# Optimization experiments

Hardware: AMD Instinct MI355X
Metric: run time of the kernel (lower is better)

Reference implementation:

```python
import jax, jax.numpy as jnp
import numpy as np

B, N, C_IN = 4, 8192, 64
NPOINT, NSAMPLE = 2048, 32
RADIUS = 0.8


def fps(xyz, npoint):
    """Furthest point sampling. xyz: (B, N, 3) -> (B, npoint) int32 indices."""
    b, n, _ = xyz.shape
    init_idx = jnp.zeros((b,), jnp.int32)
    dists0 = jnp.full((b, n), 1e10, xyz.dtype)

    def body(carry, _):
        dists, last = carry
        p = xyz[jnp.arange(b), last]                      # (B, 3) last selected point
        d = jnp.sum((xyz - p[:, None, :]) ** 2, axis=-1)  # (B, N)
        dists = jnp.minimum(dists, d)
        nxt = jnp.argmax(dists, axis=-1).astype(jnp.int32)
        return (dists, nxt), nxt

    (_, _), rest = jax.lax.scan(body, (dists0, init_idx), None, length=npoint - 1)
    return jnp.concatenate([init_idx[None, :], rest], axis=0).T  # (B, npoint)


def setup_inputs() -> dict:
    key = jax.random.key(0)
    k = jax.random.split(key, 4)
    xyz = jax.random.normal(k[0], (B, N, 3), jnp.float32) * 3.0   # point coords
    features = jax.random.normal(k[1], (B, C_IN, N), jnp.float32)
    w1 = jax.random.normal(k[2], (128, C_IN + 3), jnp.float32) * 0.05
    b1 = jnp.zeros((128,), jnp.float32)
    w2 = jax.random.normal(k[3], (256, 128), jnp.float32) * 0.05
    b2 = jnp.zeros((256,), jnp.float32)
    return {"xyz": xyz, "features": features, "w1": w1, "b1": b1, "w2": w2, "b2": b2}


def reference(xyz, features, w1, b1, w2, b2):
    b, n, _ = xyz.shape
    # --- d-fps sampling + gather_operation(new_xyz) ---
    idx_fps = fps(xyz, NPOINT)                                  # (B, S)
    new_xyz = jax.vmap(lambda p, i: p[i])(xyz, idx_fps)         # (B, S, 3)

    # --- ball query (QueryAndGroup): first NSAMPLE points within RADIUS ---
    d2 = jnp.sum((new_xyz[:, :, None, :] - xyz[:, None, :, :]) ** 2, -1)  # (B, S, N)
    in_ball = d2 < RADIUS ** 2
    idx_cnt = jnp.sum(in_ball, axis=-1)                          # (B, S)
    score = jnp.where(in_ball, jnp.arange(n, dtype=jnp.int32), n)
    neg_vals, _ = jax.lax.top_k(-score, NSAMPLE)
    idx = -neg_vals                                              # (B, S, ns) smallest valid indices
    valid = idx < n
    first = jnp.where(valid[..., :1], idx[..., :1], 0)           # pad empties with first hit (or 0)
    idx = jnp.where(valid, idx, first)

    # --- group: relative xyz concat features (use_xyz=True) ---
    gxyz = jax.vmap(lambda p, i: p[i])(xyz, idx)                 # (B, S, ns, 3)
    rel = (gxyz - new_xyz[:, :, None, :]).transpose(0, 3, 1, 2)  # (B, 3, S, ns)
    gfeat = jax.vmap(lambda f, i: f[:, i])(features, idx)        # (B, C, S, ns)
    g = jnp.concatenate([rel, gfeat], axis=1)                    # (B, C+3, S, ns)
    g = g * (idx_cnt > 0).astype(g.dtype)[:, None, :, None]      # zero empty balls

    # --- shared point MLP (1x1 conv stack) + max pool over samples ---
    h = jax.nn.relu(jnp.einsum('oc,bcsn->bosn', w1, g) + b1[None, :, None, None])
    h = jax.nn.relu(jnp.einsum('oc,bcsn->bosn', w2, h) + b2[None, :, None, None])
    pooled = jnp.max(h, axis=-1)                                 # (B, 256, S)
    return new_xyz, pooled
```

## Files before the change

### kernel.cpp

```cpp
#include <hip/hip_runtime.h>

#define NPTS   8192
#define NPT    2048
#define NS     32
#define CIN    64
#define BATCH  4
#define R2     0.64f

__global__ __launch_bounds__(256) void prep_kernel(const float* __restrict__ w1,
                                                   const float* __restrict__ w2,
                                                   float* __restrict__ w1t,
                                                   float* __restrict__ w2t) {
  int i = blockIdx.x * 256 + threadIdx.x;
  if (i < 128 * 67) {
    int o = i / 67, c = i % 67;
    w1t[c * 128 + o] = w1[i];
  }
  if (i < 256 * 128) {
    int o = i >> 7, c = i & 127;
    w2t[c * 256 + o] = w2[i];
  }
}

__global__ __launch_bounds__(256) void prep_t_kernel(const float* __restrict__ feat,
                                                     float* __restrict__ FT) {
  const int b = blockIdx.x >> 7;
  const int n0 = (blockIdx.x & 127) << 6;
  const int tid = threadIdx.x;
  __shared__ float T[64][65];

  const float* F = feat + (size_t)b * CIN * NPTS;
#pragma unroll
  for (int p = 0; p < 16; ++p) {
    int c = p * 4 + (tid >> 6), ln = tid & 63;
    T[c][ln] = F[(size_t)c * NPTS + n0 + ln];
  }
  __syncthreads();
  float* O = FT + (size_t)b * NPTS * CIN;
#pragma unroll
  for (int p = 0; p < 4; ++p) {
    int j = tid >> 2, q = (tid & 3) + p * 4;
    float4 v = make_float4(T[q * 4 + 0][j], T[q * 4 + 1][j],
                           T[q * 4 + 2][j], T[q * 4 + 3][j]);
    *(float4*)&O[(size_t)(n0 + j) * CIN + q * 4] = v;
  }
}

__device__ inline uint32_t part1by2(uint32_t x) {
  x &= 1023u;
  x = (x | (x << 16)) & 0x030000FFu;
  x = (x | (x << 8))  & 0x0300F00Fu;
  x = (x | (x << 4))  & 0x030C30C3u;
  x = (x | (x << 2))  & 0x09249249u;
  return x;
}

__device__ inline uint32_t morton3(float x, float y, float z) {
  int qx = (int)((x + 16.f) * 32.f);
  int qy = (int)((y + 16.f) * 32.f);
  int qz = (int)((z + 16.f) * 32.f);
  qx = qx < 0 ? 0 : (qx > 1023 ? 1023 : qx);
  qy = qy < 0 ? 0 : (qy > 1023 ? 1023 : qy);
  qz = qz < 0 ? 0 : (qz > 1023 ? 1023 : qz);
  return part1by2((uint32_t)qx) | (part1by2((uint32_t)qy) << 1) | (part1by2((uint32_t)qz) << 2);
}

__global__ __launch_bounds__(1024) void sort_kernel(const float* __restrict__ xyz,
                                                    float4* __restrict__ sorted) {
  const int b = blockIdx.x;
  const int tid = threadIdx.x;
  const float* X = xyz + (size_t)b * NPTS * 3;
  __shared__ uint32_t S[NPTS];

  for (int k = 0; k < 8; ++k) {
    int p = tid + (k << 10);
    uint32_t m = morton3(X[p * 3 + 0], X[p * 3 + 1], X[p * 3 + 2]);
    S[p] = ((m >> 11) << 13) | (uint32_t)p;
  }
  __syncthreads();
  for (unsigned k = 2; k <= NPTS; k <<= 1) {
    for (unsigned j = k >> 1; j > 0; j >>= 1) {
      for (int i = tid; i < NPTS; i += 1024) {
        int l = i ^ (int)j;
        if (l > i) {
          uint32_t a = S[i], c = S[l];
          bool sw = ((i & k) == 0) ? (a > c) : (a < c);
          if (sw) { S[i] = c; S[l] = a; }
        }
      }
      __syncthreads();
    }
  }
  for (int k = 0; k < 8; ++k) {
    int pos = tid + (k << 10);
    int o = (int)(S[pos] & 8191u);
    float4 v;
    v.x = X[o * 3 + 0]; v.y = X[o * 3 + 1]; v.z = X[o * 3 + 2];
    v.w = __int_as_float(o);
    sorted[(size_t)b * NPTS + pos] = v;
  }
}


#define DPP_ROR_U32_MAX(v)                                                       \
  {                                                                              \
    uint32_t _t;                                                                 \
    _t = (uint32_t)__builtin_amdgcn_update_dpp(0, (int)(v), 0x121, 0xF, 0xF, false); if (_t > (v)) (v) = _t; \
    _t = (uint32_t)__builtin_amdgcn_update_dpp(0, (int)(v), 0x122, 0xF, 0xF, false); if (_t > (v)) (v) = _t; \
    _t = (uint32_t)__builtin_amdgcn_update_dpp(0, (int)(v), 0x124, 0xF, 0xF, false); if (_t > (v)) (v) = _t; \
    _t = (uint32_t)__builtin_amdgcn_update_dpp(0, (int)(v), 0x128, 0xF, 0xF, false); if (_t > (v)) (v) = _t; \
  }

#define DPP_ROR_U32_MIN(v)                                                       \
  {                                                                              \
    uint32_t _t;                                                                 \
    _t = (uint32_t)__builtin_amdgcn_update_dpp(-1, (int)(v), 0x121, 0xF, 0xF, false); if (_t < (v)) (v) = _t; \
    _t = (uint32_t)__builtin_amdgcn_update_dpp(-1, (int)(v), 0x122, 0xF, 0xF, false); if (_t < (v)) (v) = _t; \
    _t = (uint32_t)__builtin_amdgcn_update_dpp(-1, (int)(v), 0x124, 0xF, 0xF, false); if (_t < (v)) (v) = _t; \
    _t = (uint32_t)__builtin_amdgcn_update_dpp(-1, (int)(v), 0x128, 0xF, 0xF, false); if (_t < (v)) (v) = _t; \
  }

#define CSWAP(i, j)                                                              \
  if (oid[i] > oid[j]) {                                                         \
    int _ti = oid[i]; oid[i] = oid[j]; oid[j] = _ti;                             \
    float _tf;                                                                   \
    _tf = px[i]; px[i] = px[j]; px[j] = _tf;                                     \
    _tf = py[i]; py[i] = py[j]; py[j] = _tf;                                     \
    _tf = pz[i]; pz[i] = pz[j]; pz[j] = _tf;                                     \
  }

__global__ __launch_bounds__(1024) void fps_kernel(const float* __restrict__ xyz,
                                                   const float4* __restrict__ sorted,
                                                   float* __restrict__ new_xyz) {
  const int b = blockIdx.x;
  const int tid = threadIdx.x;
  const int lane = tid & 63;
  const int wv = tid >> 6;
  const float* X = xyz + (size_t)b * NPTS * 3;
  const float4* SP = sorted + (size_t)b * NPTS;

  __shared__ float XL[NPTS * 3];
  __shared__ __align__(8) uint2 rec[2][16];

  for (int i = tid; i < NPTS * 3; i += 1024) XL[i] = X[i];

  float px[8], py[8], pz[8], dmin[8];
  int oid[8];
#pragma unroll
  for (int k = 0; k < 8; ++k) {
    float4 p = SP[tid * 8 + k];
    px[k] = p.x; py[k] = p.y; pz[k] = p.z;
    oid[k] = __float_as_int(p.w);
    dmin[k] = 1e10f;
  }
  CSWAP(0, 1) CSWAP(2, 3) CSWAP(4, 5) CSWAP(6, 7)
  CSWAP(0, 2) CSWAP(1, 3) CSWAP(4, 6) CSWAP(5, 7)
  CSWAP(1, 2) CSWAP(5, 6)
  CSWAP(0, 4) CSWAP(1, 5) CSWAP(2, 6) CSWAP(3, 7)
  CSWAP(2, 4) CSWAP(3, 5)
  CSWAP(1, 2) CSWAP(3, 4) CSWAP(5, 6)

  float bxmin = px[0], bxmax = px[0], bymin = py[0], bymax = py[0], bzmin = pz[0], bzmax = pz[0];
#pragma unroll
  for (int k = 1; k < 8; ++k) {
    bxmin = fminf(bxmin, px[k]); bxmax = fmaxf(bxmax, px[k]);
    bymin = fminf(bymin, py[k]); bymax = fmaxf(bymax, py[k]);
    bzmin = fminf(bzmin, pz[k]); bzmax = fmaxf(bzmax, pz[k]);
  }
  float cmaxv = 1e10f;
  int   cmaxi = oid[0];
  uint32_t wwm = 0u, wwi = 0u;

  float cx = X[0], cy = X[1], cz = X[2];
  if (tid == 0) {
    new_xyz[(size_t)b * NPT * 3 + 0] = cx;
    new_xyz[(size_t)b * NPT * 3 + 1] = cy;
    new_xyz[(size_t)b * NPT * 3 + 2] = cz;
  }
  __syncthreads();

  for (int t = 1; t < NPT; ++t) {
    float ex = fmaxf(fmaxf(bxmin - cx, cx - bxmax), 0.f);
    float ey = fmaxf(fmaxf(bymin - cy, cy - bymax), 0.f);
    float ez = fmaxf(fmaxf(bzmin - cz, cz - bzmax), 0.f);
    float dlb = (ex * ex + ey * ey + ez * ez) * 0.9999f;
    bool act = dlb < cmaxv;

    if (__ballot(act)) {
      if (act) {
        float mv = -1.0f; int mi = 0;
#pragma unroll
        for (int k = 0; k < 8; ++k) {
          float dx = px[k] - cx, dy = py[k] - cy, dz = pz[k] - cz;
          float d = __fadd_rn(__fadd_rn(__fmul_rn(dx, dx), __fmul_rn(dy, dy)), __fmul_rn(dz, dz));
          float dm = fminf(dmin[k], d);
          dmin[k] = dm;
          if (dm > mv) { mv = dm; mi = oid[k]; }
        }
        cmaxv = mv; cmaxi = mi;
      }
      uint32_t vb = __float_as_uint(cmaxv);
      uint32_t rm = vb;
      DPP_ROR_U32_MAX(rm)
      uint32_t m0 = (uint32_t)__builtin_amdgcn_readlane((int)rm, 0);
      uint32_t m1 = (uint32_t)__builtin_amdgcn_readlane((int)rm, 16);
      uint32_t m2 = (uint32_t)__builtin_amdgcn_readlane((int)rm, 32);
      uint32_t m3 = (uint32_t)__builtin_amdgcn_readlane((int)rm, 48);
      uint32_t wm = m0 > m1 ? m0 : m1;
      uint32_t wmb = m2 > m3 ? m2 : m3;
      wm = wm > wmb ? wm : wmb;
      unsigned long long em = __ballot(vb == wm);
      uint32_t wi;
      if (__popcll(em) == 1) {
        wi = (uint32_t)__builtin_amdgcn_readlane(cmaxi, __ffsll(em) - 1);
      } else {
        uint32_t ik = (vb == wm) ? (uint32_t)cmaxi : 0xFFFFFFFFu;
        DPP_ROR_U32_MIN(ik)
        uint32_t i0 = (uint32_t)__builtin_amdgcn_readlane((int)ik, 0);
        uint32_t i1 = (uint32_t)__builtin_amdgcn_readlane((int)ik, 16);
        uint32_t i2 = (uint32_t)__builtin_amdgcn_readlane((int)ik, 32);
        uint32_t i3 = (uint32_t)__builtin_amdgcn_readlane((int)ik, 48);
        wi = i0 < i1 ? i0 : i1;
        uint32_t wib = i2 < i3 ? i2 : i3;
        wi = wi < wib ? wi : wib;
      }
      wwm = wm; wwi = wi;
    }

    const int buf = t & 1;
    if (lane == 0) { rec[buf][wv].x = wwm; rec[buf][wv].y = wwi; }
    __syncthreads();

    uint2 r = rec[buf][lane & 15];
    uint32_t bm = r.x;
    DPP_ROR_U32_MAX(bm)
    uint32_t ci = (r.x == bm) ? r.y : 0xFFFFFFFFu;
    DPP_ROR_U32_MIN(ci)
    int sidx = __builtin_amdgcn_readfirstlane((int)ci);

    cx = XL[3 * sidx + 0];
    cy = XL[3 * sidx + 1];
    cz = XL[3 * sidx + 2];

    if (tid == 0) {
      float* o = new_xyz + ((size_t)b * NPT + t) * 3;
      o[0] = cx; o[1] = cy; o[2] = cz;
    }
  }
}

__global__ __launch_bounds__(256) void ballquery_kernel(const float* __restrict__ xyz,
                                                        const float* __restrict__ new_xyz,
                                                        int* __restrict__ idx_out) {
  const int w = blockIdx.x * 4 + (threadIdx.x >> 6);
  const int lane = threadIdx.x & 63;
  const int b = w >> 11;
  const float* X = xyz + (size_t)b * NPTS * 3;
  const float cx = new_xyz[w * 3 + 0];
  const float cy = new_xyz[w * 3 + 1];
  const float cz = new_xyz[w * 3 + 2];
  int* out = idx_out + (size_t)w * NS;

  int found = 0;
  int first = -1;
  for (int base = 0; base < NPTS; base += 64) {
    const int p = base + lane;
    float x = X[p * 3 + 0], y = X[p * 3 + 1], z = X[p * 3 + 2];
    float dx = x - cx, dy = y - cy, dz = z - cz;
    float d2 = __fadd_rn(__fadd_rn(__fmul_rn(dx, dx), __fmul_rn(dy, dy)), __fmul_rn(dz, dz));
    unsigned long long mask = __ballot(d2 < R2);
    if (mask != 0ull && first < 0) first = base + __ffsll((unsigned long long)mask) - 1;
    if (found < NS) {
      if ((mask >> lane) & 1ull) {
        int rank = found + __popcll(mask & ((1ull << lane) - 1ull));
        if (rank < NS) out[rank] = p;
      }
    }
    found += __popcll(mask);
    if (found >= NS) break;
  }
  if (found < NS) {
    int pad = (first < 0) ? 0 : first;
    if (lane >= found && lane < NS) out[lane] = pad;
  }
}

__global__ __launch_bounds__(512) void group_mlp_kernel(const float* __restrict__ xyz,
                                                        const float* __restrict__ FT,
                                                        const float* __restrict__ new_xyz,
                                                        const int* __restrict__ idx,
                                                        const float* __restrict__ w1t,
                                                        const float* __restrict__ b1,
                                                        const float* __restrict__ w2t,
                                                        const float* __restrict__ b2,
                                                        float* __restrict__ pooled) {
  const int blk = blockIdx.x;
  const int b = blk >> 10;
  const int sin0 = (2 * blk) & 2047;
  const int tid = threadIdx.x;

  __shared__ __align__(16) float G[67 * 64];
  __shared__ __align__(16) float H1[128 * 64];
  __shared__ int   lidx[2 * NS];
  __shared__ float ctr[6];

  if (tid < 64) lidx[tid] = idx[(size_t)(2 * blk) * NS + tid];
  if (tid < 6)  ctr[tid] = new_xyz[(size_t)(2 * blk) * 3 + tid];
  __syncthreads();

  const float* Fp = FT + (size_t)b * NPTS * CIN;
  const float* X = xyz + (size_t)b * NPTS * 3;

  {
    int j = tid >> 3, q = tid & 7;
    int p = lidx[j];
    const float4* row = (const float4*)(Fp + (size_t)p * CIN);
    float4 v0 = row[q * 2 + 0];
    float4 v1 = row[q * 2 + 1];
    float vs[8] = {v0.x, v0.y, v0.z, v0.w, v1.x, v1.y, v1.z, v1.w};
#pragma unroll
    for (int i = 0; i < 8; ++i)
      G[(3 + q * 8 + i) * 64 + j] = vs[i];
  }
  if (tid < 192) {
    int c = tid >> 6, j = tid & 63;
    int p = lidx[j];
    G[c * 64 + j] = X[p * 3 + c] - ctr[(j >> 5) * 3 + c];
  }
  __syncthreads();

  {
    const int oi = tid >> 4, ji = tid & 15;
    const int o0 = oi * 4, j0 = ji * 4;
    float acc[4][4];
#pragma unroll
    for (int i = 0; i < 4; ++i)
#pragma unroll
      for (int jj = 0; jj < 4; ++jj) acc[i][jj] = 0.f;
#pragma unroll 4
    for (int c = 0; c < 67; ++c) {
      float4 g  = *(const float4*)&G[c * 64 + j0];
      float4 wf = *(const float4*)&w1t[c * 128 + o0];
      float ga[4] = {g.x, g.y, g.z, g.w};
      float wa[4] = {wf.x, wf.y, wf.z, wf.w};
#pragma unroll
      for (int i = 0; i < 4; ++i)
#pragma unroll
        for (int jj = 0; jj < 4; ++jj)
          acc[i][jj] = fmaf(wa[i], ga[jj], acc[i][jj]);
    }
    float4 bb = *(const float4*)&b1[o0];
    float ba[4] = {bb.x, bb.y, bb.z, bb.w};
#pragma unroll
    for (int i = 0; i < 4; ++i) {
      float4 h;
      h.x = fmaxf(acc[i][0] + ba[i], 0.f);
      h.y = fmaxf(acc[i][1] + ba[i], 0.f);
      h.z = fmaxf(acc[i][2] + ba[i], 0.f);
      h.w = fmaxf(acc[i][3] + ba[i], 0.f);
      *(float4*)&H1[(o0 + i) * 64 + j0] = h;
    }
  }
  __syncthreads();

  {
    const int oi = tid >> 4, ji = tid & 15;
    const int o0 = oi * 8, j0 = ji * 4;
    float acc[8][4];
#pragma unroll
    for (int i = 0; i < 8; ++i)
#pragma unroll
      for (int jj = 0; jj < 4; ++jj) acc[i][jj] = 0.f;
#pragma unroll 2
    for (int c = 0; c < 128; ++c) {
      float4 h  = *(const float4*)&H1[c * 64 + j0];
      float4 wa4 = *(const float4*)&w2t[c * 256 + o0];
      float4 wb4 = *(const float4*)&w2t[c * 256 + o0 + 4];
      float ha[4] = {h.x, h.y, h.z, h.w};
      float wa[8] = {wa4.x, wa4.y, wa4.z, wa4.w, wb4.x, wb4.y, wb4.z, wb4.w};
#pragma unroll
      for (int i = 0; i < 8; ++i)
#pragma unroll
        for (int jj = 0; jj < 4; ++jj)
          acc[i][jj] = fmaf(wa[i], ha[jj], acc[i][jj]);
    }
    float4 b2a = *(const float4*)&b2[o0];
    float4 b2b = *(const float4*)&b2[o0 + 4];
    float bb[8] = {b2a.x, b2a.y, b2a.z, b2a.w, b2b.x, b2b.y, b2b.z, b2b.w};
    float m[8];
#pragma unroll
    for (int i = 0; i < 8; ++i) {
      float v0 = fmaxf(acc[i][0] + bb[i], 0.f);
      float v1 = fmaxf(acc[i][1] + bb[i], 0.f);
      float v2 = fmaxf(acc[i][2] + bb[i], 0.f);
      float v3 = fmaxf(acc[i][3] + bb[i], 0.f);
      m[i] = fmaxf(fmaxf(v0, v1), fmaxf(v2, v3));
    }
#pragma unroll
    for (int off = 1; off < 8; off <<= 1)
#pragma unroll
      for (int i = 0; i < 8; ++i) m[i] = fmaxf(m[i], __shfl_xor(m[i], off));
    const int ji_ = tid & 15;
    if (ji_ == 0 || ji_ == 8) {
      int sidx = sin0 + (ji_ >> 3);
#pragma unroll
      for (int i = 0; i < 8; ++i)
        pooled[((size_t)b * 256 + o0 + i) * (size_t)NPT + sidx] = m[i];
    }
  }
}

extern "C" void kernel_launch(void* const* d_in, const int* in_sizes, int n_in,
                              void* d_out, int out_size, void* d_ws, size_t ws_size,
                              hipStream_t stream) {
  (void)in_sizes; (void)n_in; (void)out_size; (void)ws_size;
  const float* xyz  = (const float*)d_in[0];
  const float* feat = (const float*)d_in[1];
  const float* w1   = (const float*)d_in[2];
  const float* b1   = (const float*)d_in[3];
  const float* w2   = (const float*)d_in[4];
  const float* b2   = (const float*)d_in[5];

  float* out     = (float*)d_out;
  float* new_xyz = out;
  float* pooled  = out + (size_t)BATCH * NPT * 3;

  char* ws = (char*)d_ws;
  float*  w1t    = (float*)ws;
  float*  w2t    = (float*)(ws + 34304);
  int*    idx    = (int*)(ws + 34304 + 131072);
  float4* sorted = (float4*)(ws + 1213952);
  float*  FT     = (float*)(ws + 1738240);

  prep_kernel<<<128, 256, 0, stream>>>(w1, w2, w1t, w2t);
  prep_t_kernel<<<BATCH * 128, 256, 0, stream>>>(feat, FT);
  sort_kernel<<<BATCH, 1024, 0, stream>>>(xyz, sorted);
  fps_kernel<<<BATCH, 1024, 0, stream>>>(xyz, sorted, new_xyz);
  ballquery_kernel<<<(BATCH * NPT) / 4, 256, 0, stream>>>(xyz, new_xyz, idx);
  group_mlp_kernel<<<(BATCH * NPT) / 2, 512, 0, stream>>>(xyz, FT, new_xyz, idx,
                                                          w1t, b1, w2t, b2, pooled);
}
```

Measured before the change: 1.923 ms.

## Fuse FPS, ball query and MLP into persistent kernel with progress flags

Replaces the separate FPS, ball-query and group-MLP kernels with one persistent kernel. Four blocks run FPS and publish progress every 16 samples through release atomics. The other 252 worker blocks poll those counters, then do ball query and the MLP for groups of 4 centroids, so this work overlaps the serial FPS loop. The design relies on all 256 blocks being co-resident (one 1024-thread block per CU), and the spin-waits plus the larger per-block tile add risk and can change occupancy.

```diff
diff --git a/kernel.cpp b/kernel.cpp
--- a/kernel.cpp
+++ b/kernel.cpp
@@ -6,6 +6,9 @@
 #define CIN    64
 #define BATCH  4
 #define R2     0.64f
+
+#define NWORK  252
+#define NQUAD  2048
 
 __global__ __launch_bounds__(256) void prep_kernel(const float* __restrict__ w1,
                                                    const float* __restrict__ w2,
@@ -129,283 +132,281 @@
     _tf = pz[i]; pz[i] = pz[j]; pz[j] = _tf;                                     \
   }
 
-__global__ __launch_bounds__(1024) void fps_kernel(const float* __restrict__ xyz,
-                                                   const float4* __restrict__ sorted,
-                                                   float* __restrict__ new_xyz) {
-  const int b = blockIdx.x;
+__global__ __launch_bounds__(1024, 1) void fused_kernel(
+    const float* __restrict__ xyz, const float4* __restrict__ sorted,
+    const float* __restrict__ FT,
+    const float* __restrict__ w1t, const float* __restrict__ b1,
+    const float* __restrict__ w2t, const float* __restrict__ b2,
+    float* __restrict__ new_xyz, float* __restrict__ pooled,
+    int* __restrict__ progress) {
   const int tid = threadIdx.x;
   const int lane = tid & 63;
   const int wv = tid >> 6;
-  const float* X = xyz + (size_t)b * NPTS * 3;
-  const float4* SP = sorted + (size_t)b * NPTS;
-
-  __shared__ float XL[NPTS * 3];
-  __shared__ __align__(8) uint2 rec[2][16];
-
-  for (int i = tid; i < NPTS * 3; i += 1024) XL[i] = X[i];
-
-  float px[8], py[8], pz[8], dmin[8];
-  int oid[8];
-#pragma unroll
-  for (int k = 0; k < 8; ++k) {
-    float4 p = SP[tid * 8 + k];
-    px[k] = p.x; py[k] = p.y; pz[k] = p.z;
-    oid[k] = __float_as_int(p.w);
-    dmin[k] = 1e10f;
-  }
-  CSWAP(0, 1) CSWAP(2, 3) CSWAP(4, 5) CSWAP(6, 7)
-  CSWAP(0, 2) CSWAP(1, 3) CSWAP(4, 6) CSWAP(5, 7)
-  CSWAP(1, 2) CSWAP(5, 6)
-  CSWAP(0, 4) CSWAP(1, 5) CSWAP(2, 6) CSWAP(3, 7)
-  CSWAP(2, 4) CSWAP(3, 5)
-  CSWAP(1, 2) CSWAP(3, 4) CSWAP(5, 6)
-
-  float bxmin = px[0], bxmax = px[0], bymin = py[0], bymax = py[0], bzmin = pz[0], bzmax = pz[0];
-#pragma unroll
-  for (int k = 1; k < 8; ++k) {
-    bxmin = fminf(bxmin, px[k]); bxmax = fmaxf(bxmax, px[k]);
-    bymin = fminf(bymin, py[k]); bymax = fmaxf(bymax, py[k]);
-    bzmin = fminf(bzmin, pz[k]); bzmax = fmaxf(bzmax, pz[k]);
-  }
-  float cmaxv = 1e10f;
-  int   cmaxi = oid[0];
-  uint32_t wwm = 0u, wwi = 0u;
-
-  float cx = X[0], cy = X[1], cz = X[2];
-  if (tid == 0) {
-    new_xyz[(size_t)b * NPT * 3 + 0] = cx;
-    new_xyz[(size_t)b * NPT * 3 + 1] = cy;
-    new_xyz[(size_t)b * NPT * 3 + 2] = cz;
-  }
-  __syncthreads();
-
-  for (int t = 1; t < NPT; ++t) {
-    float ex = fmaxf(fmaxf(bxmin - cx, cx - bxmax), 0.f);
-    float ey = fmaxf(fmaxf(bymin - cy, cy - bymax), 0.f);
-    float ez = fmaxf(fmaxf(bzmin - cz, cz - bzmax), 0.f);
-    float dlb = (ex * ex + ey * ey + ez * ez) * 0.9999f;
-    bool act = dlb < cmaxv;
-
-    if (__ballot(act)) {
-      if (act) {
-        float mv = -1.0f; int mi = 0;
-#pragma unroll
-        for (int k = 0; k < 8; ++k) {
-          float dx = px[k] - cx, dy = py[k] - cy, dz = pz[k] - cz;
-          float d = __fadd_rn(__fadd_rn(__fmul_rn(dx, dx), __fmul_rn(dy, dy)), __fmul_rn(dz, dz));
-          float dm = fminf(dmin[k], d);
-          dmin[k] = dm;
-          if (dm > mv) { mv = dm; mi = oid[k]; }
-        }
-        cmaxv = mv; cmaxi = mi;
-      }
-      uint32_t vb = __float_as_uint(cmaxv);
-      uint32_t rm = vb;
-      DPP_ROR_U32_MAX(rm)
-      uint32_t m0 = (uint32_t)__builtin_amdgcn_readlane((int)rm, 0);
-      uint32_t m1 = (uint32_t)__builtin_amdgcn_readlane((int)rm, 16);
-      uint32_t m2 = (uint32_t)__builtin_amdgcn_readlane((int)rm, 32);
-      uint32_t m3 = (uint32_t)__builtin_amdgcn_readlane((int)rm, 48);
-      uint32_t wm = m0 > m1 ? m0 : m1;
-      uint32_t wmb = m2 > m3 ? m2 : m3;
-      wm = wm > wmb ? wm : wmb;
-      unsigned long long em = __ballot(vb == wm);
-      uint32_t wi;
-      if (__popcll(em) == 1) {
-        wi = (uint32_t)__builtin_amdgcn_readlane(cmaxi, __ffsll(em) - 1);
-      } else {
-        uint32_t ik = (vb == wm) ? (uint32_t)cmaxi : 0xFFFFFFFFu;
-        DPP_ROR_U32_MIN(ik)
-        uint32_t i0 = (uint32_t)__builtin_amdgcn_readlane((int)ik, 0);
-        uint32_t i1 = (uint32_t)__builtin_amdgcn_readlane((int)ik, 16);
-        uint32_t i2 = (uint32_t)__builtin_amdgcn_readlane((int)ik, 32);
-        uint32_t i3 = (uint32_t)__builtin_amdgcn_readlane((int)ik, 48);
-        wi = i0 < i1 ? i0 : i1;
-        uint32_t wib = i2 < i3 ? i2 : i3;
-        wi = wi < wib ? wi : wib;
-      }
-      wwm = wm; wwi = wi;
-    }
-
-    const int buf = t & 1;
-    if (lane == 0) { rec[buf][wv].x = wwm; rec[buf][wv].y = wwi; }
+
+  __shared__ __align__(16) char SM[100416];
+
+  if (blockIdx.x < 4) {
+    const int b = blockIdx.x;
+    float* XL = (float*)SM;
+    uint2 (*rec)[16] = (uint2(*)[16])(SM + 98304);
+    const float* X = xyz + (size_t)b * NPTS * 3;
+    const float4* SP = sorted + (size_t)b * NPTS;
+
+    for (int i = tid; i < NPTS * 3; i += 1024) XL[i] = X[i];
+
+    float px[8], py[8], pz[8], dmin[8];
+    int oid[8];
+#pragma unroll
+    for (int k = 0; k < 8; ++k) {
+      float4 p = SP[tid * 8 + k];
+      px[k] = p.x; py[k] = p.y; pz[k] = p.z;
+      oid[k] = __float_as_int(p.w);
+      dmin[k] = 1e10f;
+    }
+    CSWAP(0, 1) CSWAP(2, 3) CSWAP(4, 5) CSWAP(6, 7)
+    CSWAP(0, 2) CSWAP(1, 3) CSWAP(4, 6) CSWAP(5, 7)
+    CSWAP(1, 2) CSWAP(5, 6)
+    CSWAP(0, 4) CSWAP(1, 5) CSWAP(2, 6) CSWAP(3, 7)
+    CSWAP(2, 4) CSWAP(3, 5)
+    CSWAP(1, 2) CSWAP(3, 4) CSWAP(5, 6)
+
+    float bxmin = px[0], bxmax = px[0], bymin = py[0], bymax = py[0], bzmin = pz[0], bzmax = pz[0];
+#pragma unroll
+    for (int k = 1; k < 8; ++k) {
+      bxmin = fminf(bxmin, px[k]); bxmax = fmaxf(bxmax, px[k]);
+      bymin = fminf(bymin, py[k]); bymax = fmaxf(bymax, py[k]);
+      bzmin = fminf(bzmin, pz[k]); bzmax = fmaxf(bzmax, pz[k]);
+    }
+    float cmaxv = 1e10f;
+    int   cmaxi = oid[0];
+    uint32_t wwm = 0u, wwi = 0u;
+
+    float cx = X[0], cy = X[1], cz = X[2];
+    if (tid == 0) {
+      new_xyz[(size_t)b * NPT * 3 + 0] = cx;
+      new_xyz[(size_t)b * NPT * 3 + 1] = cy;
+      new_xyz[(size_t)b * NPT * 3 + 2] = cz;
+    }
     __syncthreads();
 
-    uint2 r = rec[buf][lane & 15];
-    uint32_t bm = r.x;
-    DPP_ROR_U32_MAX(bm)
-    uint32_t ci = (r.x == bm) ? r.y : 0xFFFFFFFFu;
-    DPP_ROR_U32_MIN(ci)
-    int sidx = __builtin_amdgcn_readfirstlane((int)ci);
-
-    cx = XL[3 * sidx + 0];
-    cy = XL[3 * sidx + 1];
-    cz = XL[3 * sidx + 2];
-
-    if (tid == 0) {
-      float* o = new_xyz + ((size_t)b * NPT + t) * 3;
-      o[0] = cx; o[1] = cy; o[2] = cz;
-    }
-  }
-}
-
-__global__ __launch_bounds__(256) void ballquery_kernel(const float* __restrict__ xyz,
-                                                        const float* __restrict__ new_xyz,
-                                                        int* __restrict__ idx_out) {
-  const int w = blockIdx.x * 4 + (threadIdx.x >> 6);
-  const int lane = threadIdx.x & 63;
-  const int b = w >> 11;
-  const float* X = xyz + (size_t)b * NPTS * 3;
-  const float cx = new_xyz[w * 3 + 0];
-  const float cy = new_xyz[w * 3 + 1];
-  const float cz = new_xyz[w * 3 + 2];
-  int* out = idx_out + (size_t)w * NS;
-
-  int found = 0;
-  int first = -1;
-  for (int base = 0; base < NPTS; base += 64) {
-    const int p = base + lane;
-    float x = X[p * 3 + 0], y = X[p * 3 + 1], z = X[p * 3 + 2];
-    float dx = x - cx, dy = y - cy, dz = z - cz;
-    float d2 = __fadd_rn(__fadd_rn(__fmul_rn(dx, dx), __fmul_rn(dy, dy)), __fmul_rn(dz, dz));
-    unsigned long long mask = __ballot(d2 < R2);
-    if (mask != 0ull && first < 0) first = base + __ffsll((unsigned long long)mask) - 1;
-    if (found < NS) {
-      if ((mask >> lane) & 1ull) {
-        int rank = found + __popcll(mask & ((1ull << lane) - 1ull));
-        if (rank < NS) out[rank] = p;
-      }
-    }
-    found += __popcll(mask);
-    if (found >= NS) break;
-  }
-  if (found < NS) {
-    int pad = (first < 0) ? 0 : first;
-    if (lane >= found && lane < NS) out[lane] = pad;
-  }
-}
-
-__global__ __launch_bounds__(512) void group_mlp_kernel(const float* __restrict__ xyz,
-                                                        const float* __restrict__ FT,
-                                                        const float* __restrict__ new_xyz,
-                                                        const int* __restrict__ idx,
-                                                        const float* __restrict__ w1t,
-                                                        const float* __restrict__ b1,
-                                                        const float* __restrict__ w2t,
-                                                        const float* __restrict__ b2,
-                                                        float* __restrict__ pooled) {
-  const int blk = blockIdx.x;
-  const int b = blk >> 10;
-  const int sin0 = (2 * blk) & 2047;
-  const int tid = threadIdx.x;
-
-  __shared__ __align__(16) float G[67 * 64];
-  __shared__ __align__(16) float H1[128 * 64];
-  __shared__ int   lidx[2 * NS];
-  __shared__ float ctr[6];
-
-  if (tid < 64) lidx[tid] = idx[(size_t)(2 * blk) * NS + tid];
-  if (tid < 6)  ctr[tid] = new_xyz[(size_t)(2 * blk) * 3 + tid];
-  __syncthreads();
-
-  const float* Fp = FT + (size_t)b * NPTS * CIN;
-  const float* X = xyz + (size_t)b * NPTS * 3;
-
-  {
-    int j = tid >> 3, q = tid & 7;
-    int p = lidx[j];
-    const float4* row = (const float4*)(Fp + (size_t)p * CIN);
-    float4 v0 = row[q * 2 + 0];
-    float4 v1 = row[q * 2 + 1];
-    float vs[8] = {v0.x, v0.y, v0.z, v0.w, v1.x, v1.y, v1.z, v1.w};
-#pragma unroll
-    for (int i = 0; i < 8; ++i)
-      G[(3 + q * 8 + i) * 64 + j] = vs[i];
-  }
-  if (tid < 192) {
-    int c = tid >> 6, j = tid & 63;
-    int p = lidx[j];
-    G[c * 64 + j] = X[p * 3 + c] - ctr[(j >> 5) * 3 + c];
-  }
-  __syncthreads();
-
-  {
-    const int oi = tid >> 4, ji = tid & 15;
-    const int o0 = oi * 4, j0 = ji * 4;
-    float acc[4][4];
-#pragma unroll
-    for (int i = 0; i < 4; ++i)
-#pragma unroll
-      for (int jj = 0; jj < 4; ++jj) acc[i][jj] = 0.f;
+    for (int t = 1; t < NPT; ++t) {
+      float ex = fmaxf(fmaxf(bxmin - cx, cx - bxmax), 0.f);
+      float ey = fmaxf(fmaxf(bymin - cy, cy - bymax), 0.f);
+      float ez = fmaxf(fmaxf(bzmin - cz, cz - bzmax), 0.f);
+      float dlb = (ex * ex + ey * ey + ez * ez) * 0.9999f;
+      bool act = dlb < cmaxv;
+
+      if (__ballot(act)) {
+        if (act) {
+          float mv = -1.0f; int mi = 0;
+#pragma unroll
+          for (int k = 0; k < 8; ++k) {
+            float dx = px[k] - cx, dy = py[k] - cy, dz = pz[k] - cz;
+            float d = __fadd_rn(__fadd_rn(__fmul_rn(dx, dx), __fmul_rn(dy, dy)), __fmul_rn(dz, dz));
+            float dm = fminf(dmin[k], d);
+            dmin[k] = dm;
+            if (dm > mv) { mv = dm; mi = oid[k]; }
+          }
+          cmaxv = mv; cmaxi = mi;
+        }
+        uint32_t vb = __float_as_uint(cmaxv);
+        uint32_t rm = vb;
+        DPP_ROR_U32_MAX(rm)
+        uint32_t m0 = (uint32_t)__builtin_amdgcn_readlane((int)rm, 0);
+        uint32_t m1 = (uint32_t)__builtin_amdgcn_readlane((int)rm, 16);
+        uint32_t m2 = (uint32_t)__builtin_amdgcn_readlane((int)rm, 32);
+        uint32_t m3 = (uint32_t)__builtin_amdgcn_readlane((int)rm, 48);
+        uint32_t wm = m0 > m1 ? m0 : m1;
+        uint32_t wmb = m2 > m3 ? m2 : m3;
+        wm = wm > wmb ? wm : wmb;
+        unsigned long long em = __ballot(vb == wm);
+        uint32_t wi;
+        if (__popcll(em) == 1) {
+          wi = (uint32_t)__builtin_amdgcn_readlane(cmaxi, __ffsll(em) - 1);
+        } else {
+          uint32_t ik = (vb == wm) ? (uint32_t)cmaxi : 0xFFFFFFFFu;
+          DPP_ROR_U32_MIN(ik)
+          uint32_t i0 = (uint32_t)__builtin_amdgcn_readlane((int)ik, 0);
+          uint32_t i1 = (uint32_t)__builtin_amdgcn_readlane((int)ik, 16);
+          uint32_t i2 = (uint32_t)__builtin_amdgcn_readlane((int)ik, 32);
+          uint32_t i3 = (uint32_t)__builtin_amdgcn_readlane((int)ik, 48);
+          wi = i0 < i1 ? i0 : i1;
+          uint32_t wib = i2 < i3 ? i2 : i3;
+          wi = wi < wib ? wi : wib;
+        }
+        wwm = wm; wwi = wi;
+      }
+
+      const int buf = t & 1;
+      if (lane == 0) { rec[buf][wv].x = wwm; rec[buf][wv].y = wwi; }
+      __syncthreads();
+
+      uint2 r = rec[buf][lane & 15];
+      uint32_t bm = r.x;
+      DPP_ROR_U32_MAX(bm)
+      uint32_t ci = (r.x == bm) ? r.y : 0xFFFFFFFFu;
+      DPP_ROR_U32_MIN(ci)
+      int sidx = __builtin_amdgcn_readfirstlane((int)ci);
+
+      cx = XL[3 * sidx + 0];
+      cy = XL[3 * sidx + 1];
+      cz = XL[3 * sidx + 2];
+
+      if (tid == 0) {
+        float* o = new_xyz + ((size_t)b * NPT + t) * 3;
+        o[0] = cx; o[1] = cy; o[2] = cz;
+        if ((t & 15) == 15)
+          __hip_atomic_store(progress + b, t, __ATOMIC_RELEASE, __HIP_MEMORY_SCOPE_AGENT);
+      }
+    }
+  } else {
+    float* G    = (float*)SM;
+    float* H1   = (float*)(SM + 34304);
+    int*   lidx = (int*)(SM + 99840);
+    float* ctr  = (float*)(SM + 100352);
+
+    const int wbid = blockIdx.x - 4;
+
+    for (int qg = wbid; qg < NQUAD; qg += NWORK) {
+      const int b = qg & 3;
+      const int s0 = (qg >> 2) * 4;
+      const float* X  = xyz + (size_t)b * NPTS * 3;
+      const float* Fp = FT + (size_t)b * NPTS * CIN;
+
+      if (tid == 0) {
+        while (__hip_atomic_load(progress + b, __ATOMIC_ACQUIRE, __HIP_MEMORY_SCOPE_AGENT) < s0 + 3)
+          __builtin_amdgcn_s_sleep(2);
+      }
+      __syncthreads();
+
+      if (tid < 12) ctr[tid] = new_xyz[((size_t)b * NPT + s0) * 3 + tid];
+      if (wv < 4) {
+        const int s = s0 + wv;
+        const float cx = new_xyz[((size_t)b * NPT + s) * 3 + 0];
+        const float cy = new_xyz[((size_t)b * NPT + s) * 3 + 1];
+        const float cz = new_xyz[((size_t)b * NPT + s) * 3 + 2];
+        int* out = lidx + wv * NS;
+        int found = 0;
+        int first = -1;
+        for (int base = 0; base < NPTS; base += 64) {
+          const int p = base + lane;
+          float x = X[p * 3 + 0], y = X[p * 3 + 1], z = X[p * 3 + 2];
+          float dx = x - cx, dy = y - cy, dz = z - cz;
+          float d2 = __fadd_rn(__fadd_rn(__fmul_rn(dx, dx), __fmul_rn(dy, dy)), __fmul_rn(dz, dz));
+          unsigned long long mask = __ballot(d2 < R2);
+          if (mask != 0ull && first < 0) first = base + __ffsll((unsigned long long)mask) - 1;
+          if (found < NS) {
+            if ((mask >> lane) & 1ull) {
+              int rank = found + __popcll(mask & ((1ull << lane) - 1ull));
+              if (rank < NS) out[rank] = p;
+            }
+          }
+          found += __popcll(mask);
+          if (found >= NS) break;
+        }
+        if (found < NS) {
+          int pad = (first < 0) ? 0 : first;
+          if (lane >= found && lane < NS) out[lane] = pad;
+        }
+      }
+      __syncthreads();
+
+      {
+        int j = tid >> 3, q = tid & 7;
+        int p = lidx[j];
+        const float4* row = (const float4*)(Fp + (size_t)p * CIN);
+        float4 v0 = row[q * 2 + 0];
+        float4 v1 = row[q * 2 + 1];
+        float vs[8] = {v0.x, v0.y, v0.z, v0.w, v1.x, v1.y, v1.z, v1.w};
+#pragma unroll
+        for (int i = 0; i < 8; ++i)
+          G[(3 + q * 8 + i) * 128 + j] = vs[i];
+      }
+      if (tid < 384) {
+        int c = tid >> 7, j = tid & 127;
+        int p = lidx[j];
+        G[c * 128 + j] = X[p * 3 + c] - ctr[(j >> 5) * 3 + c];
+      }
+      __syncthreads();
+
+      {
+        const int oi = tid >> 5, ji = tid & 31;
+        const int o0 = oi * 4, j0 = ji * 4;
+        float acc[4][4];
+#pragma unroll
+        for (int i = 0; i < 4; ++i)
+#pragma unroll
+          for (int jj = 0; jj < 4; ++jj) acc[i][jj] = 0.f;
 #pragma unroll 4
-    for (int c = 0; c < 67; ++c) {
-      float4 g  = *(const float4*)&G[c * 64 + j0];
-      float4 wf = *(const float4*)&w1t[c * 128 + o0];
-      float ga[4] = {g.x, g.y, g.z, g.w};
-      float wa[4] = {wf.x, wf.y, wf.z, wf.w};
-#pragma unroll
-      for (int i = 0; i < 4; ++i)
-#pragma unroll
-        for (int jj = 0; jj < 4; ++jj)
-          acc[i][jj] = fmaf(wa[i], ga[jj], acc[i][jj]);
-    }
-    float4 bb = *(const float4*)&b1[o0];
-    float ba[4] = {bb.x, bb.y, bb.z, bb.w};
-#pragma unroll
-    for (int i = 0; i < 4; ++i) {
-      float4 h;
-      h.x = fmaxf(acc[i][0] + ba[i], 0.f);
-      h.y = fmaxf(acc[i][1] + ba[i], 0.f);
-      h.z = fmaxf(acc[i][2] + ba[i], 0.f);
-      h.w = fmaxf(acc[i][3] + ba[i], 0.f);
-      *(float4*)&H1[(o0 + i) * 64 + j0] = h;
-    }
-  }
-  __syncthreads();
-
-  {
-    const int oi = tid >> 4, ji = tid & 15;
-    const int o0 = oi * 8, j0 = ji * 4;
-    float acc[8][4];
-#pragma unroll
-    for (int i = 0; i < 8; ++i)
-#pragma unroll
-      for (int jj = 0; jj < 4; ++jj) acc[i][jj] = 0.f;
+        for (int c = 0; c < 67; ++c) {
+          float4 g  = *(const float4*)&G[c * 128 + j0];
+          float4 wf = *(const float4*)&w1t[c * 128 + o0];
+          float ga[4] = {g.x, g.y, g.z, g.w};
+          float wa[4] = {wf.x, wf.y, wf.z, wf.w};
+#pragma unroll
+          for (int i = 0; i < 4; ++i)
+#pragma unroll
+            for (int jj = 0; jj < 4; ++jj)
+              acc[i][jj] = fmaf(wa[i], ga[jj], acc[i][jj]);
+        }
+        float4 bb = *(const float4*)&b1[o0];
+        float ba[4] = {bb.x, bb.y, bb.z, bb.w};
+#pragma unroll
+        for (int i = 0; i < 4; ++i) {
+          float4 h;
+          h.x = fmaxf(acc[i][0] + ba[i], 0.f);
+          h.y = fmaxf(acc[i][1] + ba[i], 0.f);
+          h.z = fmaxf(acc[i][2] + ba[i], 0.f);
+          h.w = fmaxf(acc[i][3] + ba[i], 0.f);
+          *(float4*)&H1[(o0 + i) * 128 + j0] = h;
+        }
+      }
+      __syncthreads();
+
+      {
+        const int oi = tid >> 5, ji = tid & 31;
+        const int o0 = oi * 8, j0 = ji * 4;
+        float acc[8][4];
+#pragma unroll
+        for (int i = 0; i < 8; ++i)
+#pragma unroll
+          for (int jj = 0; jj < 4; ++jj) acc[i][jj] = 0.f;
 #pragma unroll 2
-    for (int c = 0; c < 128; ++c) {
-      float4 h  = *(const float4*)&H1[c * 64 + j0];
-      float4 wa4 = *(const float4*)&w2t[c * 256 + o0];
-      float4 wb4 = *(const float4*)&w2t[c * 256 + o0 + 4];
-      float ha[4] = {h.x, h.y, h.z, h.w};
-      float wa[8] = {wa4.x, wa4.y, wa4.z, wa4.w, wb4.x, wb4.y, wb4.z, wb4.w};
-#pragma unroll
-      for (int i = 0; i < 8; ++i)
-#pragma unroll
-        for (int jj = 0; jj < 4; ++jj)
-          acc[i][jj] = fmaf(wa[i], ha[jj], acc[i][jj]);
-    }
-    float4 b2a = *(const float4*)&b2[o0];
-    float4 b2b = *(const float4*)&b2[o0 + 4];
-    float bb[8] = {b2a.x, b2a.y, b2a.z, b2a.w, b2b.x, b2b.y, b2b.z, b2b.w};
-    float m[8];
-#pragma unroll
-    for (int i = 0; i < 8; ++i) {
-      float v0 = fmaxf(acc[i][0] + bb[i], 0.f);
-      float v1 = fmaxf(acc[i][1] + bb[i], 0.f);
-      float v2 = fmaxf(acc[i][2] + bb[i], 0.f);
-      float v3 = fmaxf(acc[i][3] + bb[i], 0.f);
-      m[i] = fmaxf(fmaxf(v0, v1), fmaxf(v2, v3));
-    }
-#pragma unroll
-    for (int off = 1; off < 8; off <<= 1)
-#pragma unroll
-      for (int i = 0; i < 8; ++i) m[i] = fmaxf(m[i], __shfl_xor(m[i], off));
-    const int ji_ = tid & 15;
-    if (ji_ == 0 || ji_ == 8) {
-      int sidx = sin0 + (ji_ >> 3);
-#pragma unroll
-      for (int i = 0; i < 8; ++i)
-        pooled[((size_t)b * 256 + o0 + i) * (size_t)NPT + sidx] = m[i];
+        for (int c = 0; c < 128; ++c) {
+          float4 h  = *(const float4*)&H1[c * 128 + j0];
+          float4 wa4 = *(const float4*)&w2t[c * 256 + o0];
+          float4 wb4 = *(const float4*)&w2t[c * 256 + o0 + 4];
+          float ha[4] = {h.x, h.y, h.z, h.w};
+          float wa[8] = {wa4.x, wa4.y, wa4.z, wa4.w, wb4.x, wb4.y, wb4.z, wb4.w};
+#pragma unroll
+          for (int i = 0; i < 8; ++i)
+#pragma unroll
+            for (int jj = 0; jj < 4; ++jj)
+              acc[i][jj] = fmaf(wa[i], ha[jj], acc[i][jj]);
+        }
+        float4 b2a = *(const float4*)&b2[o0];
+        float4 b2b = *(const float4*)&b2[o0 + 4];
+        float bb[8] = {b2a.x, b2a.y, b2a.z, b2a.w, b2b.x, b2b.y, b2b.z, b2b.w};
+        float m[8];
+#pragma unroll
+        for (int i = 0; i < 8; ++i) {
+          float v0 = fmaxf(acc[i][0] + bb[i], 0.f);
+          float v1 = fmaxf(acc[i][1] + bb[i], 0.f);
+          float v2 = fmaxf(acc[i][2] + bb[i], 0.f);
+          float v3 = fmaxf(acc[i][3] + bb[i], 0.f);
+          m[i] = fmaxf(fmaxf(v0, v1), fmaxf(v2, v3));
+        }
+#pragma unroll
+        for (int off = 1; off < 8; off <<= 1)
+#pragma unroll
+          for (int i = 0; i < 8; ++i) m[i] = fmaxf(m[i], __shfl_xor(m[i], off));
+        if ((ji & 7) == 0) {
+          int sidx = s0 + (ji >> 3);
+#pragma unroll
+          for (int i = 0; i < 8; ++i)
+            pooled[((size_t)b * 256 + o0 + i) * (size_t)NPT + sidx] = m[i];
+        }
+      }
     }
   }
 }
@@ -426,17 +427,16 @@
   float* pooled  = out + (size_t)BATCH * NPT * 3;
 
   char* ws = (char*)d_ws;
-  float*  w1t    = (float*)ws;
-  float*  w2t    = (float*)(ws + 34304);
-  int*    idx    = (int*)(ws + 34304 + 131072);
-  float4* sorted = (float4*)(ws + 1213952);
-  float*  FT     = (float*)(ws + 1738240);
+  float*  w1t      = (float*)ws;
+  float*  w2t      = (float*)(ws + 34304);
+  float4* sorted   = (float4*)(ws + 165376);
+  float*  FT       = (float*)(ws + 689664);
+  int*    progress = (int*)(ws + 9078272);
 
   prep_kernel<<<128, 256, 0, stream>>>(w1, w2, w1t, w2t);
   prep_t_kernel<<<BATCH * 128, 256, 0, stream>>>(feat, FT);
   sort_kernel<<<BATCH, 1024, 0, stream>>>(xyz, sorted);
-  fps_kernel<<<BATCH, 1024, 0, stream>>>(xyz, sorted, new_xyz);
-  ballquery_kernel<<<(BATCH * NPT) / 4, 256, 0, stream>>>(xyz, new_xyz, idx);
-  group_mlp_kernel<<<(BATCH * NPT) / 2, 512, 0, stream>>>(xyz, FT, new_xyz, idx,
-                                                          w1t, b1, w2t, b2, pooled);
-}
+  (void)hipMemsetAsync(progress, 0, 16, stream);
+  fused_kernel<<<256, 1024, 0, stream>>>(xyz, sorted, FT, w1t, b1, w2t, b2,
+                                         new_xyz, pooled, progress);
+}
```

Result: faster. 1.687 ms (-12.3%).
